# Optimization experiments

Hardware: AMD Instinct MI355X
Metric: run time of the kernel (lower is better)

## Reference

```python
import jax, jax.numpy as jnp
import numpy as np

B, T, C = 2, 2048, 1024
H, D = 16, 64
EPS = 1e-6


def _layernorm(x, gamma, beta):
    # Faithful to the torch module: uses unbiased std (Bessel) and divides by (std + eps).
    mean = x.mean(-1, keepdims=True)
    std = jnp.sqrt(jnp.sum((x - mean) ** 2, axis=-1, keepdims=True) / (x.shape[-1] - 1))
    return gamma * (x - mean) / (std + EPS) + beta


def setup_inputs() -> dict:
    key = jax.random.key(0)
    ks = jax.random.split(key, 9)
    s = lambda fan_in: 1.0 / np.sqrt(fan_in)
    return {
        "x": jax.random.normal(ks[0], (B, T, C), dtype=jnp.float32),
        "qkv_w": jax.random.uniform(ks[1], (3 * C, C), jnp.float32, -s(C), s(C)),
        "proj_w": jax.random.uniform(ks[2], (C, C), jnp.float32, -s(C), s(C)),
        "proj_b": jax.random.uniform(ks[3], (C,), jnp.float32, -s(C), s(C)),
        "l1_w": jax.random.uniform(ks[4], (4 * C, C), jnp.float32, -s(C), s(C)),
        "l1_b": jax.random.uniform(ks[5], (4 * C,), jnp.float32, -s(C), s(C)),
        "l3_w": jax.random.uniform(ks[6], (C, 4 * C), jnp.float32, -s(4 * C), s(4 * C)),
        "l3_b": jax.random.uniform(ks[7], (C,), jnp.float32, -s(4 * C), s(4 * C)),
        "ln1_g": jnp.ones((C,), jnp.float32),
        "ln1_b": jnp.zeros((C,), jnp.float32),
        "ln2_g": jnp.ones((C,), jnp.float32),
        "ln2_b": jnp.zeros((C,), jnp.float32),
    }


def _attention(x, qkv_w, proj_w, proj_b):
    Bx, Tx, Cx = x.shape
    qkv = x @ qkv_w.T                      # [B,T,3C]
    q, k, v = jnp.split(qkv, 3, axis=-1)
    q = q.reshape(Bx, Tx, H, D)
    k = k.reshape(Bx, Tx, H, D)
    v = v.reshape(Bx, Tx, H, D)
    scores = jnp.einsum("bthd,bshd->bhts", q, k) * (D ** -0.5)  # [B,H,T,T]
    causal = jnp.tril(jnp.ones((Tx, Tx), dtype=bool))
    scores = jnp.where(causal, scores, -jnp.inf)
    attn = jax.nn.softmax(scores, axis=-1)
    out = jnp.einsum("bhts,bshd->bthd", attn, v).reshape(Bx, Tx, Cx)
    return out @ proj_w.T + proj_b


def _mlp(x, l1_w, l1_b, l3_w, l3_b):
    h = jax.nn.relu(x @ l1_w.T + l1_b)     # [B,T,4C]
    return h @ l3_w.T + l3_b


def reference(x, qkv_w, proj_w, proj_b, l1_w, l1_b, l3_w, l3_b, ln1_g, ln1_b, ln2_g, ln2_b):
    # Dropout is identity in eval mode.
    x1 = x + _attention(_layernorm(x, ln1_g, ln1_b), qkv_w, proj_w, proj_b)
    x2 = x1 + _mlp(_layernorm(x1, ln2_g, ln2_b), l1_w, l1_b, l3_w, l3_b)
    return x2
```

## Files before the change

kernel.cpp:

```cpp
#include <hip/hip_runtime.h>

typedef unsigned short u16;
typedef short short8 __attribute__((ext_vector_type(8)));
typedef float floatx4 __attribute__((ext_vector_type(4)));

#define TT 2048
#define CC 1024
#define QSCALE 0.1803368801111244f
#define MFIX 32.0f

__device__ __forceinline__ u16 f2bf(float f) {
  return (u16)((__float_as_uint(f) + 0x8000u) >> 16);
}

__device__ __forceinline__ unsigned int pk2bf(float a, float b) {
  unsigned int ua = __float_as_uint(a) + 0x8000u;
  unsigned int ub = __float_as_uint(b) + 0x8000u;
  return __builtin_amdgcn_perm(ub, ua, 0x07060302u);
}

__device__ __forceinline__ void glds16(const u16* g, u16* l) {
  __builtin_amdgcn_global_load_lds((const __attribute__((address_space(1))) void*)g,
                                   (__attribute__((address_space(3))) void*)l, 16, 0, 0);
}

__device__ __forceinline__ void ln_body(const float* __restrict__ x,
                                        const float* __restrict__ g,
                                        const float* __restrict__ b,
                                        u16* __restrict__ out, int row, int tid) {
  const float4* xr = (const float4*)(x + (size_t)row * CC);
  float4 v = xr[tid];
  float s = v.x + v.y + v.z + v.w;
  float sq = v.x * v.x + v.y * v.y + v.z * v.z + v.w * v.w;
#pragma unroll
  for (int off = 1; off < 64; off <<= 1) {
    s += __shfl_xor(s, off);
    sq += __shfl_xor(sq, off);
  }
  __shared__ float ss[4], ssq[4];
  int wave = tid >> 6;
  if ((tid & 63) == 0) { ss[wave] = s; ssq[wave] = sq; }
  __syncthreads();
  s = ss[0] + ss[1] + ss[2] + ss[3];
  sq = ssq[0] + ssq[1] + ssq[2] + ssq[3];
  float mean = s * (1.0f / CC);
  float var = (sq - (float)CC * mean * mean) * (1.0f / (CC - 1));
  float inv = 1.0f / (sqrtf(fmaxf(var, 0.0f)) + 1e-6f);
  float4 gv = ((const float4*)g)[tid];
  float4 bv = ((const float4*)b)[tid];
  ushort4 o;
  o.x = f2bf(gv.x * (v.x - mean) * inv + bv.x);
  o.y = f2bf(gv.y * (v.y - mean) * inv + bv.y);
  o.z = f2bf(gv.z * (v.z - mean) * inv + bv.z);
  o.w = f2bf(gv.w * (v.w - mean) * inv + bv.w);
  ((ushort4*)(out + (size_t)row * CC))[tid] = o;
}

__global__ __launch_bounds__(256) void cvt_ln_kernel(const float* __restrict__ w0,
                                                     const float* __restrict__ w1,
                                                     const float* __restrict__ w2,
                                                     const float* __restrict__ w3,
                                                     const float* __restrict__ x,
                                                     const float* __restrict__ lg,
                                                     const float* __restrict__ lb,
                                                     u16* __restrict__ o0,
                                                     u16* __restrict__ o1,
                                                     u16* __restrict__ o2,
                                                     u16* __restrict__ o3,
                                                     u16* __restrict__ oln) {
  int blk = blockIdx.x;
  if (blk >= 12288) {
    ln_body(x, lg, lb, oln, blk - 12288, threadIdx.x);
    return;
  }
  const float* in;
  u16* out;
  int base;
  if (blk < 3072)      { in = w0; out = o0; base = 0; }
  else if (blk < 4096) { in = w1; out = o1; base = 3072; }
  else if (blk < 8192) { in = w2; out = o2; base = 4096; }
  else                 { in = w3; out = o3; base = 8192; }
  int i = (blk - base) * 256 + threadIdx.x;
  float4 v = ((const float4*)in)[i];
  ushort4 o;
  o.x = f2bf(v.x); o.y = f2bf(v.y); o.z = f2bf(v.z); o.w = f2bf(v.w);
  ((ushort4*)out)[i] = o;
}

__global__ __launch_bounds__(256) void ln_kernel(const float* __restrict__ x,
                                                 const float* __restrict__ g,
                                                 const float* __restrict__ b,
                                                 u16* __restrict__ out) {
  ln_body(x, g, b, out, blockIdx.x, threadIdx.x);
}


#define STAGE(tt)                                                         \
  {                                                                       \
    _Pragma("unroll") for (int g_ = 0; g_ < G; g_++)                      \
        glds16(gptr[g_] + (size_t)(tt) * 64, &lds[(tt) % RING][ldd[g_]]); \
  }

#define BODY(t, VM)                                                       \
  {                                                                       \
    asm volatile("s_waitcnt vmcnt(" #VM ")" ::: "memory");                \
    __builtin_amdgcn_s_barrier();                                         \
    asm volatile("" ::: "memory");                                        \
    if ((t) + DEPTH < nst) STAGE((t) + DEPTH);                            \
    const u16* Ls = &lds[(t) % RING][0];                                  \
    _Pragma("unroll") for (int s_ = 0; s_ < 2; s_++) {                    \
      short8 bf[NJ];                                                      \
      _Pragma("unroll") for (int j_ = 0; j_ < NJ; j_++)                   \
          bf[j_] = *(const short8*)(Ls + (bOff[j_] ^ (s_ << 5)));         \
      _Pragma("unroll") for (int h_ = 0; h_ < MH; h_++) {                 \
        short8 af[MC];                                                    \
        _Pragma("unroll") for (int m_ = 0; m_ < MC; m_++)                 \
            af[m_] = *(const short8*)(Ls + (aOff[h_ * MC + m_] ^ (s_ << 5))); \
        if (MIDB && (s_ + h_ > 0)) __builtin_amdgcn_s_barrier();          \
        __builtin_amdgcn_s_setprio(1);                                    \
        _Pragma("unroll") for (int m_ = 0; m_ < MC; m_++)                 \
            _Pragma("unroll") for (int j_ = 0; j_ < NJ; j_++)             \
                acc[h_ * MC + m_][j_] = __builtin_amdgcn_mfma_f32_16x16x32_bf16( \
                    af[m_], bf[j_], acc[h_ * MC + m_][j_], 0, 0, 0);      \
        __builtin_amdgcn_s_setprio(0);                                    \
      }                                                                   \
    }                                                                     \
  }

template <int BM, int BN, int NWM, int NWN, int MODE, int DEPTH>
__global__ __launch_bounds__(64 * NWM * NWN, 2) void gemmp(
    const u16* __restrict__ A, const u16* __restrict__ W,
    const float* __restrict__ bias, const float* __restrict__ resid,
    float* __restrict__ outf, u16* __restrict__ outb,
    int M, int N, int K) {
  constexpr int NW = NWM * NWN;
  constexpr int MI = BM / NWM / 16;
  constexpr int NJ = BN / NWN / 16;
  constexpr int ROWS = BM + BN;
  constexpr int G = ROWS / 8 / NW;
  constexpr int MH = (MI > 4) ? 2 : 1;
  constexpr int MC = MI / MH;
  constexpr int RING = DEPTH + 1;
  constexpr bool MIDB = (NW == 8);
  static_assert(ROWS % (8 * NW) == 0, "chunk assignment");
  static_assert(DEPTH == 1 || G == 6, "counted vmcnt literal assumes G==6");
  __shared__ u16 lds[RING][ROWS * 64];

  const int tid = threadIdx.x;
  const int w = tid >> 6, lane = tid & 63;
  const int l15 = lane & 15, quad = lane >> 4;
  const int wm = (w / NWN) * (MI * 16);
  const int wn = (w % NWN) * (NJ * 16);
  const int tm = blockIdx.x * BM, tn = blockIdx.y * BN;

  const int srow = lane >> 3;
  const int xk = (lane & 7) ^ srow;
  const u16* gptr[G];
  int ldd[G];
#pragma unroll
  for (int g = 0; g < G; g++) {
    int c8 = (g * NW + w) * 8;
    const u16* rb = (c8 < BM) ? (A + (size_t)(tm + c8) * K)
                              : (W + (size_t)(tn + c8 - BM) * K);
    gptr[g] = rb + (size_t)srow * K + xk * 8;
    ldd[g] = c8 * 64;
  }

  int aOff[MI], bOff[NJ];
#pragma unroll
  for (int m = 0; m < MI; m++)
    aOff[m] = (wm + m * 16 + l15) * 64 + ((quad ^ (l15 & 7)) * 8);
#pragma unroll
  for (int j = 0; j < NJ; j++)
    bOff[j] = (BM + wn + j * 16 + l15) * 64 + ((quad ^ (l15 & 7)) * 8);

  floatx4 acc[MI][NJ];
#pragma unroll
  for (int m = 0; m < MI; m++)
#pragma unroll
    for (int j = 0; j < NJ; j++) acc[m][j] = (floatx4){0.f, 0.f, 0.f, 0.f};

  const int nst = K >> 6;

  STAGE(0);
  if constexpr (DEPTH == 2) STAGE(1);

  if constexpr (DEPTH == 1) {
#pragma unroll 2
    for (int t = 0; t < nst; ++t) BODY(t, 0);
  } else {
#pragma unroll 3
    for (int t = 0; t < nst - 1; ++t) BODY(t, 6);
    BODY(nst - 1, 0);
  }

  float bb[NJ];
#pragma unroll
  for (int j = 0; j < NJ; j++)
    bb[j] = (MODE == 1 || MODE == 2) ? bias[tn + wn + j * 16 + l15] : 0.0f;
#pragma unroll
  for (int m = 0; m < MI; m++) {
    int row0 = tm + wm + m * 16 + quad * 4;
#pragma unroll
    for (int j = 0; j < NJ; j++) {
      int col = tn + wn + j * 16 + l15;
#pragma unroll
      for (int r = 0; r < 4; r++) {
        float v = acc[m][j][r];
        size_t idx = (size_t)(row0 + r) * N + col;
        if (MODE == 0) {
          if (col < 1024) v *= QSCALE;
          outb[idx] = f2bf(v);
        } else if (MODE == 1) {
          outf[idx] = v + bb[j] + resid[idx];
        } else {
          outb[idx] = f2bf(fmaxf(v + bb[j], 0.0f));
        }
      }
    }
  }
}

#undef STAGE
#undef BODY


#define STG32(tt)                                                         \
  {                                                                       \
    _Pragma("unroll") for (int g_ = 0; g_ < 4; g_++)                      \
        glds16(gptr[g_] + (size_t)(tt) * 32, &lds[(tt) & 3][ldd[g_]]);    \
  }

#define BODY32(t, VM)                                                     \
  {                                                                       \
    asm volatile("s_waitcnt vmcnt(" #VM ")" ::: "memory");                \
    __builtin_amdgcn_s_barrier();                                         \
    asm volatile("" ::: "memory");                                        \
    if ((t) + 3 < nst) STG32((t) + 3);                                    \
    const u16* Ls = &lds[(t) & 3][0];                                     \
    short8 bf[4];                                                         \
    _Pragma("unroll") for (int j_ = 0; j_ < 4; j_++)                      \
        bf[j_] = *(const short8*)(Ls + bOff[j_]);                         \
    _Pragma("unroll") for (int h_ = 0; h_ < 4; h_++) {                    \
      short8 a0_ = *(const short8*)(Ls + aOff[2 * h_]);                   \
      short8 a1_ = *(const short8*)(Ls + aOff[2 * h_ + 1]);               \
      if (h_ > 0) __builtin_amdgcn_s_barrier();                           \
      __builtin_amdgcn_s_setprio(1);                                      \
      _Pragma("unroll") for (int j_ = 0; j_ < 4; j_++)                    \
          acc[2 * h_][j_] = __builtin_amdgcn_mfma_f32_16x16x32_bf16(      \
              a0_, bf[j_], acc[2 * h_][j_], 0, 0, 0);                     \
      _Pragma("unroll") for (int j_ = 0; j_ < 4; j_++)                    \
          acc[2 * h_ + 1][j_] = __builtin_amdgcn_mfma_f32_16x16x32_bf16(  \
              a1_, bf[j_], acc[2 * h_ + 1][j_], 0, 0, 0);                 \
      __builtin_amdgcn_s_setprio(0);                                      \
    }                                                                     \
  }

template <int MODE>
__global__ __launch_bounds__(512, 2) void gemm32(const u16* __restrict__ A,
                                                 const u16* __restrict__ W,
                                                 const float* __restrict__ bias,
                                                 u16* __restrict__ outb,
                                                 int M, int N, int K) {
  __shared__ u16 lds[4][512 * 32];
  const int tid = threadIdx.x;
  const int w = tid >> 6, lane = tid & 63;
  const int l15 = lane & 15, quad = lane >> 4;
  const int wm = (w >> 2) * 128, wn = (w & 3) * 64;
  const int tm = blockIdx.x * 256, tn = blockIdx.y * 256;

  const int srow = lane >> 2;
  const int xk = (lane & 3) ^ ((lane >> 3) & 3);
  const u16* gptr[4];
  int ldd[4];
#pragma unroll
  for (int g = 0; g < 4; g++) {
    int c16 = (g * 8 + w) * 16;
    const u16* rb = (c16 < 256) ? (A + (size_t)(tm + c16) * K)
                                : (W + (size_t)(tn + c16 - 256) * K);
    gptr[g] = rb + (size_t)srow * K + xk * 8;
    ldd[g] = c16 * 32;
  }

  const int rsw = (quad ^ ((l15 >> 1) & 3)) * 8;
  int aOff[8], bOff[4];
#pragma unroll
  for (int m = 0; m < 8; m++) aOff[m] = (wm + m * 16 + l15) * 32 + rsw;
#pragma unroll
  for (int j = 0; j < 4; j++) bOff[j] = (256 + wn + j * 16 + l15) * 32 + rsw;

  floatx4 acc[8][4];
#pragma unroll
  for (int m = 0; m < 8; m++)
#pragma unroll
    for (int j = 0; j < 4; j++) acc[m][j] = (floatx4){0.f, 0.f, 0.f, 0.f};

  const int nst = K >> 5;

  STG32(0);
  STG32(1);
  STG32(2);

#pragma unroll 4
  for (int t = 0; t < nst - 2; ++t) BODY32(t, 8);
  BODY32(nst - 2, 4);
  BODY32(nst - 1, 0);

  float bb[4];
#pragma unroll
  for (int j = 0; j < 4; j++)
    bb[j] = (MODE == 2) ? bias[tn + wn + j * 16 + l15] : 0.0f;
#pragma unroll
  for (int m = 0; m < 8; m++) {
    int row0 = tm + wm + m * 16 + quad * 4;
#pragma unroll
    for (int j = 0; j < 4; j++) {
      int col = tn + wn + j * 16 + l15;
#pragma unroll
      for (int r = 0; r < 4; r++) {
        float v = acc[m][j][r];
        size_t idx = (size_t)(row0 + r) * N + col;
        if (MODE == 0) {
          if (col < 1024) v *= QSCALE;
          outb[idx] = f2bf(v);
        } else {
          outb[idx] = f2bf(fmaxf(v + bb[j], 0.0f));
        }
      }
    }
  }
}

#undef STG32
#undef BODY32

__global__ __launch_bounds__(256) void flash_kernel(const u16* __restrict__ qkv,
                                                    u16* __restrict__ attn) {
  int bid = blockIdx.x;
  int qt = 31 - (bid >> 5);
  int bh = bid & 31;
  int b = bh >> 4, h = bh & 15;
  int tid = threadIdx.x, w = tid >> 6, lane = tid & 63;
  int l15 = lane & 15, quad = lane >> 4;

  __shared__ u16 k_lds[128 * 64];
  __shared__ u16 vt_lds[64 * 128];
  __shared__ u16 p_lds[4][16 * 128];

  int qbase = qt * 64 + w * 16;
  const u16* qp = qkv + (size_t)(b * TT + qbase + l15) * 3072 + h * 64;
  short8 qf0 = *(const short8*)(qp + quad * 8);
  short8 qf1 = *(const short8*)(qp + 32 + quad * 8);

  float l_i = 0.0f;
  floatx4 accO[4];
#pragma unroll
  for (int jf = 0; jf < 4; jf++) accO[jf] = (floatx4){0.f, 0.f, 0.f, 0.f};

  int rsub = lane >> 3;
  int cg = (lane & 7) ^ rsub;
  const u16* Kg = qkv + (size_t)(b * TT + w * 32 + rsub) * 3072 + 1024 + h * 64 + cg * 8;
  u16* kL = k_lds + w * 32 * 64;
  int s4 = (tid & 31) * 4;
  int dg = (tid >> 5) * 8;
  const u16* Vg = qkv + (size_t)(b * TT + s4) * 3072 + 2048 + h * 64 + dg;
  int sl = s4 >> 3, so = s4 & 7;

  int x = l15 & 7;
  int kOff[8];
#pragma unroll
  for (int i = 0; i < 8; i++) kOff[i] = (i * 16 + l15) * 64 + ((quad ^ x) * 8);

  int nt = (qt + 2) >> 1;
  for (int kt = 0; kt < nt; kt++) {
    int s0 = kt * 128;
    size_t soff = (size_t)s0 * 3072;
    uint4 R0 = *(const uint4*)(Vg + soff);
    uint4 R1 = *(const uint4*)(Vg + soff + 3072);
    uint4 R2 = *(const uint4*)(Vg + soff + 6144);
    uint4 R3 = *(const uint4*)(Vg + soff + 9216);
    __syncthreads();
#pragma unroll
    for (int is = 0; is < 4; is++) glds16(Kg + soff + (size_t)is * 8 * 3072, kL + is * 512);
    {
      unsigned int a0[4] = {R0.x, R0.y, R0.z, R0.w};
      unsigned int a1[4] = {R1.x, R1.y, R1.z, R1.w};
      unsigned int a2[4] = {R2.x, R2.y, R2.z, R2.w};
      unsigned int a3[4] = {R3.x, R3.y, R3.z, R3.w};
#pragma unroll
      for (int p = 0; p < 4; p++) {
        uint2 ev, od;
        ev.x = __builtin_amdgcn_perm(a1[p], a0[p], 0x05040100u);
        ev.y = __builtin_amdgcn_perm(a3[p], a2[p], 0x05040100u);
        od.x = __builtin_amdgcn_perm(a1[p], a0[p], 0x07060302u);
        od.y = __builtin_amdgcn_perm(a3[p], a2[p], 0x07060302u);
        int r0 = dg + 2 * p, r1 = r0 + 1;
        *(uint2*)(vt_lds + r0 * 128 + ((sl ^ (r0 & 15)) << 3) + so) = ev;
        *(uint2*)(vt_lds + r1 * 128 + ((sl ^ (r1 & 15)) << 3) + so) = od;
      }
    }
    __syncthreads();

    floatx4 st[8];
#pragma unroll
    for (int i = 0; i < 8; i++) st[i] = (floatx4){0.f, 0.f, 0.f, 0.f};
#pragma unroll
    for (int i = 0; i < 8; i++) {
      short8 kf0 = *(const short8*)(k_lds + kOff[i]);
      short8 kf1 = *(const short8*)(k_lds + (kOff[i] ^ 32));
      st[i] = __builtin_amdgcn_mfma_f32_16x16x32_bf16(kf0, qf0, st[i], 0, 0, 0);
      st[i] = __builtin_amdgcn_mfma_f32_16x16x32_bf16(kf1, qf1, st[i], 0, 0, 0);
    }

    if (s0 + 127 > qbase) {
      int mg = qbase + l15;
#pragma unroll
      for (int i = 0; i < 8; i++)
#pragma unroll
        for (int r = 0; r < 4; r++) {
          int s = s0 + i * 16 + quad * 4 + r;
          if (s > mg) st[i][r] = -3.0e38f;
        }
    }

    float ts = 0.0f;
#pragma unroll
    for (int i = 0; i < 8; i++)
#pragma unroll
      for (int r = 0; r < 4; r++) {
        float p = __builtin_amdgcn_exp2f(st[i][r] - MFIX);
        st[i][r] = p;
        ts += p;
      }
    ts += __shfl_xor(ts, 16);
    ts += __shfl_xor(ts, 32);
    l_i += ts;

#pragma unroll
    for (int i = 0; i < 8; i++) {
      uint2 pk;
      pk.x = pk2bf(st[i][0], st[i][1]);
      pk.y = pk2bf(st[i][2], st[i][3]);
      *(uint2*)(p_lds[w] + l15 * 128 + (((2 * i + (quad >> 1)) ^ l15) << 3) +
                ((quad & 1) << 2)) = pk;
    }

    short8 pf[4];
#pragma unroll
    for (int c = 0; c < 4; c++)
      pf[c] = *(const short8*)(p_lds[w] + l15 * 128 + (((quad + 4 * c) ^ l15) << 3));
#pragma unroll
    for (int jf = 0; jf < 4; jf++) {
      int vRow = (jf * 16 + l15) * 128;
#pragma unroll
      for (int c = 0; c < 4; c++) {
        short8 vf = *(const short8*)(vt_lds + vRow + (((quad + 4 * c) ^ l15) << 3));
        accO[jf] = __builtin_amdgcn_mfma_f32_16x16x32_bf16(pf[c], vf, accO[jf], 0, 0, 0);
      }
    }
  }

  float invl = 1.0f / l_i;
  float iR[4];
#pragma unroll
  for (int r = 0; r < 4; r++) iR[r] = __shfl(invl, quad * 4 + r);
  int orow = b * TT + qbase + quad * 4;
#pragma unroll
  for (int r = 0; r < 4; r++) {
    u16* op = attn + (size_t)(orow + r) * CC + h * 64 + l15;
#pragma unroll
    for (int jf = 0; jf < 4; jf++) op[jf * 16] = f2bf(accO[jf][r] * iR[r]);
  }
}

extern "C" void kernel_launch(void* const* d_in, const int* in_sizes, int n_in,
                              void* d_out, int out_size, void* d_ws, size_t ws_size,
                              hipStream_t stream) {
  const float* x      = (const float*)d_in[0];
  const float* qkv_w  = (const float*)d_in[1];
  const float* proj_w = (const float*)d_in[2];
  const float* proj_b = (const float*)d_in[3];
  const float* l1_w   = (const float*)d_in[4];
  const float* l1_b   = (const float*)d_in[5];
  const float* l3_w   = (const float*)d_in[6];
  const float* l3_b   = (const float*)d_in[7];
  const float* ln1_g  = (const float*)d_in[8];
  const float* ln1_b  = (const float*)d_in[9];
  const float* ln2_g  = (const float*)d_in[10];
  const float* ln2_b  = (const float*)d_in[11];
  float* out = (float*)d_out;
  char* ws = (char*)d_ws;

  u16* w_qkv  = (u16*)(ws + 0);
  u16* w_proj = (u16*)(ws + 6291456);
  u16* w_l1   = (u16*)(ws + 8388608);
  u16* w_l3   = (u16*)(ws + 16777216);
  u16* lnb    = (u16*)(ws + 25165824);
  u16* qkvb   = (u16*)(ws + 33554432);
  u16* attnb  = (u16*)(ws + 58720256);
  float* x1   = (float*)(ws + 67108864);
  u16* hb     = (u16*)(ws + 83886080);

  cvt_ln_kernel<<<16384, 256, 0, stream>>>(qkv_w, proj_w, l1_w, l3_w, x, ln1_g, ln1_b,
                                           w_qkv, w_proj, w_l1, w_l3, lnb);
  gemm32<0><<<dim3(16, 12), 512, 0, stream>>>(lnb, w_qkv, nullptr, qkvb, 4096, 3072, 1024);
  flash_kernel<<<1024, 256, 0, stream>>>(qkvb, attnb);
  gemmp<128, 64, 2, 2, 1, 2><<<dim3(32, 16), 256, 0, stream>>>(
      attnb, w_proj, proj_b, x, x1, nullptr, 4096, 1024, 1024);
  ln_kernel<<<4096, 256, 0, stream>>>(x1, ln2_g, ln2_b, lnb);
  gemm32<2><<<dim3(16, 16), 512, 0, stream>>>(lnb, w_l1, l1_b, hb, 4096, 4096, 1024);
  gemmp<128, 64, 2, 2, 1, 2><<<dim3(32, 16), 256, 0, stream>>>(
      hb, w_l3, l3_b, x1, out, nullptr, 4096, 1024, 4096);
}
```

Before: 286.2 us.

## Replace residual GEMM with K32 four-stage pipelined kernel at three blocks per CU

The proj and l3 residual GEMMs move from the generic gemmp template (K-step 64, double-buffered) to a specialized gemms kernel. It uses K-step 32 with a 4-slot LDS ring holding three stages in flight, a new XOR swizzle for 32-wide rows, and launch bounds that allow 3 blocks per CU. The goal is more latency hiding and occupancy with a smaller LDS footprint. The cost is more barriers per unit of K work and the removal of the generic template modes.

```diff
diff --git a/kernel.cpp b/kernel.cpp
--- a/kernel.cpp
+++ b/kernel.cpp
@@ -95,134 +95,103 @@
 }
 
 
-#define STAGE(tt)                                                         \
+#define STGS(tt)                                                          \
   {                                                                       \
-    _Pragma("unroll") for (int g_ = 0; g_ < G; g_++)                      \
-        glds16(gptr[g_] + (size_t)(tt) * 64, &lds[(tt) % RING][ldd[g_]]); \
-  }
-
-#define BODY(t, VM)                                                       \
+    _Pragma("unroll") for (int g_ = 0; g_ < 3; g_++)                      \
+        glds16(gptrs[g_] + (size_t)(tt) * 32, &lds[(tt) & 3][ldds[g_]]);  \
+  }
+
+#define BODYS(t, VM)                                                      \
   {                                                                       \
     asm volatile("s_waitcnt vmcnt(" #VM ")" ::: "memory");                \
     __builtin_amdgcn_s_barrier();                                         \
     asm volatile("" ::: "memory");                                        \
-    if ((t) + DEPTH < nst) STAGE((t) + DEPTH);                            \
-    const u16* Ls = &lds[(t) % RING][0];                                  \
-    _Pragma("unroll") for (int s_ = 0; s_ < 2; s_++) {                    \
-      short8 bf[NJ];                                                      \
-      _Pragma("unroll") for (int j_ = 0; j_ < NJ; j_++)                   \
-          bf[j_] = *(const short8*)(Ls + (bOff[j_] ^ (s_ << 5)));         \
-      _Pragma("unroll") for (int h_ = 0; h_ < MH; h_++) {                 \
-        short8 af[MC];                                                    \
-        _Pragma("unroll") for (int m_ = 0; m_ < MC; m_++)                 \
-            af[m_] = *(const short8*)(Ls + (aOff[h_ * MC + m_] ^ (s_ << 5))); \
-        if (MIDB && (s_ + h_ > 0)) __builtin_amdgcn_s_barrier();          \
-        __builtin_amdgcn_s_setprio(1);                                    \
-        _Pragma("unroll") for (int m_ = 0; m_ < MC; m_++)                 \
-            _Pragma("unroll") for (int j_ = 0; j_ < NJ; j_++)             \
-                acc[h_ * MC + m_][j_] = __builtin_amdgcn_mfma_f32_16x16x32_bf16( \
-                    af[m_], bf[j_], acc[h_ * MC + m_][j_], 0, 0, 0);      \
-        __builtin_amdgcn_s_setprio(0);                                    \
-      }                                                                   \
+    if ((t) + 3 < nst) STGS((t) + 3);                                     \
+    const u16* Ls = &lds[(t) & 3][0];                                     \
+    short8 bf0 = *(const short8*)(Ls + bOff[0]);                          \
+    short8 bf1 = *(const short8*)(Ls + bOff[1]);                          \
+    short8 af[4];                                                         \
+    _Pragma("unroll") for (int m_ = 0; m_ < 4; m_++)                      \
+        af[m_] = *(const short8*)(Ls + aOff[m_]);                         \
+    __builtin_amdgcn_s_setprio(1);                                        \
+    _Pragma("unroll") for (int m_ = 0; m_ < 4; m_++) {                    \
+      acc[m_][0] = __builtin_amdgcn_mfma_f32_16x16x32_bf16(af[m_], bf0, acc[m_][0], 0, 0, 0); \
+      acc[m_][1] = __builtin_amdgcn_mfma_f32_16x16x32_bf16(af[m_], bf1, acc[m_][1], 0, 0, 0); \
     }                                                                     \
-  }
-
-template <int BM, int BN, int NWM, int NWN, int MODE, int DEPTH>
-__global__ __launch_bounds__(64 * NWM * NWN, 2) void gemmp(
-    const u16* __restrict__ A, const u16* __restrict__ W,
-    const float* __restrict__ bias, const float* __restrict__ resid,
-    float* __restrict__ outf, u16* __restrict__ outb,
-    int M, int N, int K) {
-  constexpr int NW = NWM * NWN;
-  constexpr int MI = BM / NWM / 16;
-  constexpr int NJ = BN / NWN / 16;
-  constexpr int ROWS = BM + BN;
-  constexpr int G = ROWS / 8 / NW;
-  constexpr int MH = (MI > 4) ? 2 : 1;
-  constexpr int MC = MI / MH;
-  constexpr int RING = DEPTH + 1;
-  constexpr bool MIDB = (NW == 8);
-  static_assert(ROWS % (8 * NW) == 0, "chunk assignment");
-  static_assert(DEPTH == 1 || G == 6, "counted vmcnt literal assumes G==6");
-  __shared__ u16 lds[RING][ROWS * 64];
-
+    __builtin_amdgcn_s_setprio(0);                                        \
+  }
+
+template <int MODE>
+__global__ __launch_bounds__(256, 3) void gemms(const u16* __restrict__ A,
+                                                const u16* __restrict__ W,
+                                                const float* __restrict__ bias,
+                                                const float* __restrict__ resid,
+                                                float* __restrict__ outf,
+                                                int M, int N, int K) {
+  __shared__ u16 lds[4][192 * 32];
   const int tid = threadIdx.x;
   const int w = tid >> 6, lane = tid & 63;
   const int l15 = lane & 15, quad = lane >> 4;
-  const int wm = (w / NWN) * (MI * 16);
-  const int wn = (w % NWN) * (NJ * 16);
-  const int tm = blockIdx.x * BM, tn = blockIdx.y * BN;
-
-  const int srow = lane >> 3;
-  const int xk = (lane & 7) ^ srow;
-  const u16* gptr[G];
-  int ldd[G];
-#pragma unroll
-  for (int g = 0; g < G; g++) {
-    int c8 = (g * NW + w) * 8;
-    const u16* rb = (c8 < BM) ? (A + (size_t)(tm + c8) * K)
-                              : (W + (size_t)(tn + c8 - BM) * K);
-    gptr[g] = rb + (size_t)srow * K + xk * 8;
-    ldd[g] = c8 * 64;
-  }
-
-  int aOff[MI], bOff[NJ];
-#pragma unroll
-  for (int m = 0; m < MI; m++)
-    aOff[m] = (wm + m * 16 + l15) * 64 + ((quad ^ (l15 & 7)) * 8);
-#pragma unroll
-  for (int j = 0; j < NJ; j++)
-    bOff[j] = (BM + wn + j * 16 + l15) * 64 + ((quad ^ (l15 & 7)) * 8);
-
-  floatx4 acc[MI][NJ];
-#pragma unroll
-  for (int m = 0; m < MI; m++)
-#pragma unroll
-    for (int j = 0; j < NJ; j++) acc[m][j] = (floatx4){0.f, 0.f, 0.f, 0.f};
-
-  const int nst = K >> 6;
-
-  STAGE(0);
-  if constexpr (DEPTH == 2) STAGE(1);
-
-  if constexpr (DEPTH == 1) {
-#pragma unroll 2
-    for (int t = 0; t < nst; ++t) BODY(t, 0);
-  } else {
-#pragma unroll 3
-    for (int t = 0; t < nst - 1; ++t) BODY(t, 6);
-    BODY(nst - 1, 0);
-  }
-
-  float bb[NJ];
-#pragma unroll
-  for (int j = 0; j < NJ; j++)
-    bb[j] = (MODE == 1 || MODE == 2) ? bias[tn + wn + j * 16 + l15] : 0.0f;
-#pragma unroll
-  for (int m = 0; m < MI; m++) {
+  const int wm = (w >> 1) * 64, wn = (w & 1) * 32;
+  const int tm = blockIdx.x * 128, tn = blockIdx.y * 64;
+
+  const int srow = lane >> 2;
+  const int xk = (lane & 3) ^ ((lane >> 3) & 3);
+  const u16* gptrs[3];
+  int ldds[3];
+#pragma unroll
+  for (int g = 0; g < 3; g++) {
+    int c16 = (g * 4 + w) * 16;
+    const u16* rb = (c16 < 128) ? (A + (size_t)(tm + c16) * K)
+                                : (W + (size_t)(tn + c16 - 128) * K);
+    gptrs[g] = rb + (size_t)srow * K + xk * 8;
+    ldds[g] = c16 * 32;
+  }
+
+  const int rsw = (quad ^ ((l15 >> 1) & 3)) * 8;
+  int aOff[4], bOff[2];
+#pragma unroll
+  for (int m = 0; m < 4; m++) aOff[m] = (wm + m * 16 + l15) * 32 + rsw;
+#pragma unroll
+  for (int j = 0; j < 2; j++) bOff[j] = (128 + wn + j * 16 + l15) * 32 + rsw;
+
+  floatx4 acc[4][2];
+#pragma unroll
+  for (int m = 0; m < 4; m++)
+#pragma unroll
+    for (int j = 0; j < 2; j++) acc[m][j] = (floatx4){0.f, 0.f, 0.f, 0.f};
+
+  const int nst = K >> 5;
+
+  STGS(0);
+  STGS(1);
+  STGS(2);
+
+#pragma unroll 4
+  for (int t = 0; t < nst - 2; ++t) BODYS(t, 6);
+  BODYS(nst - 2, 3);
+  BODYS(nst - 1, 0);
+
+  float bb[2];
+#pragma unroll
+  for (int j = 0; j < 2; j++) bb[j] = bias[tn + wn + j * 16 + l15];
+#pragma unroll
+  for (int m = 0; m < 4; m++) {
     int row0 = tm + wm + m * 16 + quad * 4;
 #pragma unroll
-    for (int j = 0; j < NJ; j++) {
+    for (int j = 0; j < 2; j++) {
       int col = tn + wn + j * 16 + l15;
 #pragma unroll
       for (int r = 0; r < 4; r++) {
-        float v = acc[m][j][r];
         size_t idx = (size_t)(row0 + r) * N + col;
-        if (MODE == 0) {
-          if (col < 1024) v *= QSCALE;
-          outb[idx] = f2bf(v);
-        } else if (MODE == 1) {
-          outf[idx] = v + bb[j] + resid[idx];
-        } else {
-          outb[idx] = f2bf(fmaxf(v + bb[j], 0.0f));
-        }
+        outf[idx] = acc[m][j][r] + bb[j] + resid[idx];
       }
     }
   }
 }
 
-#undef STAGE
-#undef BODY
+#undef STGS
+#undef BODYS
 
 
 #define STG32(tt)                                                         \
@@ -505,10 +474,8 @@
                                            w_qkv, w_proj, w_l1, w_l3, lnb);
   gemm32<0><<<dim3(16, 12), 512, 0, stream>>>(lnb, w_qkv, nullptr, qkvb, 4096, 3072, 1024);
   flash_kernel<<<1024, 256, 0, stream>>>(qkvb, attnb);
-  gemmp<128, 64, 2, 2, 1, 2><<<dim3(32, 16), 256, 0, stream>>>(
-      attnb, w_proj, proj_b, x, x1, nullptr, 4096, 1024, 1024);
+  gemms<1><<<dim3(32, 16), 256, 0, stream>>>(attnb, w_proj, proj_b, x, x1, 4096, 1024, 1024);
   ln_kernel<<<4096, 256, 0, stream>>>(x1, ln2_g, ln2_b, lnb);
   gemm32<2><<<dim3(16, 16), 512, 0, stream>>>(lnb, w_l1, l1_b, hb, 4096, 4096, 1024);
-  gemmp<128, 64, 2, 2, 1, 2><<<dim3(32, 16), 256, 0, stream>>>(
-      hb, w_l3, l3_b, x1, out, nullptr, 4096, 1024, 4096);
-}
+  gemms<1><<<dim3(32, 16), 256, 0, stream>>>(hb, w_l3, l3_b, x1, out, 4096, 1024, 4096);
+}
```

Measured after the change: 312.3 us. 9.1% more time.
